# Performance work log

Measured on AMD Instinct MI355X. Metric: run time of the kernel, lower is better.

The kernel has to match this reference:

```python
import jax, jax.numpy as jnp
import numpy as np

B, C = 512, 65536
EPS_COS = 1e-8   # torch cosine_similarity eps
EPS_BCE = 1e-10  # SupGraphLoss denominator eps


def setup_inputs() -> dict:
    key = jax.random.key(0)
    k1, k2, k3 = jax.random.split(key, 3)
    prediction = jax.random.normal(k1, (B, C), dtype=jnp.float32)          # raw logits from the model
    # sparse multi-hot ground-truth labels (yolo_target)
    target = (jax.random.uniform(k2, (B, C)) < 0.02).astype(jnp.float32)
    has_count = jax.random.bernoulli(k3, 0.7, (C,))
    cos_weights = jnp.where(has_count, 0.5, 1.0).astype(jnp.float32)       # CosineOntLoss weights
    bce_weights = has_count.astype(jnp.float32)                            # SupGraphLoss weights
    return {"prediction": prediction, "target": target,
            "cos_weights": cos_weights, "bce_weights": bce_weights}


def _cos_cel_loss(prediction, target, cos_weights, cos_norm_w):
    # CosineOntLoss(result=target, target=prediction):
    # both scaled by weights, cosine similarity along class dim, negative mean.
    a = target * cos_weights       # "target" arg inside CosineOntLoss
    b = prediction * cos_weights   # "result" arg inside CosineOntLoss
    num = jnp.sum(a * b, axis=1)
    na = jnp.sqrt(jnp.sum(a * a, axis=1))
    nb = jnp.sqrt(jnp.sum(b * b, axis=1))
    cos = num / (jnp.maximum(na, EPS_COS) * jnp.maximum(nb, EPS_COS))
    cosine_loss = -jnp.mean(cos)

    # SupGraphLoss(result=target, target=prediction): BCEWithLogits with
    # logits = ground-truth target, soft-target = prediction (faithful to source arg order)
    x = target       # logits
    y = prediction   # bce target
    bce = jnp.maximum(x, 0.0) - x * y + jnp.log1p(jnp.exp(-jnp.abs(x)))  # stable BCEWithLogits
    sub_graph_loss = jnp.sum(bce * cos_norm_w) / (jnp.sum(cos_norm_w) + EPS_BCE)

    return cosine_loss + sub_graph_loss / 10.0


def reference(prediction, target, cos_weights, bce_weights):
    return _cos_cel_loss(prediction, target, cos_weights, bce_weights)
```

## Files before the change

kernel.cpp:

```cpp
#include <hip/hip_runtime.h>

#define B_ROWS   512
#define C_COLS   65536
#define CHUNKS   4
#define T1       256
#define T2       512

__device__ __forceinline__ void wave_reduce4(float& a, float& b, float& c, float& d) {
    #pragma unroll
    for (int off = 32; off >= 1; off >>= 1) {
        a += __shfl_down(a, off);
        b += __shfl_down(b, off);
        c += __shfl_down(c, off);
        d += __shfl_down(d, off);
    }
}

__global__ __launch_bounds__(T1) void coscel_partial(
    const float* __restrict__ pred,
    const float* __restrict__ tgt,
    const float* __restrict__ cw,
    const float* __restrict__ bw,
    float4* __restrict__ ws)
{
    const int blk   = blockIdx.x;
    const int row   = blk >> 2;
    const int chunk = blk & (CHUNKS - 1);
    const int tid   = threadIdx.x;

    const size_t base   = (size_t)row * C_COLS + (size_t)chunk * (C_COLS / CHUNKS);
    const size_t wbase  = (size_t)chunk * (C_COLS / CHUNKS);

    const float4* __restrict__ p4 = (const float4*)(pred + base);
    const float4* __restrict__ t4 = (const float4*)(tgt  + base);
    const float4* __restrict__ w4 = (const float4*)(cw   + wbase);
    const float4* __restrict__ g4 = (const float4*)(bw   + wbase);

    float num = 0.f, a2 = 0.f, b2 = 0.f, bce = 0.f;

    #pragma unroll 4
    for (int i = 0; i < 16; ++i) {
        const int idx = i * T1 + tid;
        const float4 p = p4[idx];
        const float4 t = t4[idx];
        const float4 w = w4[idx];
        const float4 g = g4[idx];

        #define DO_COMP(comp)                                              \
        {                                                                  \
            const float a = t.comp * w.comp;                               \
            const float b = p.comp * w.comp;                               \
            num += a * b;                                                  \
            a2  += a * a;                                                  \
            b2  += b * b;                                                  \
            const float x = t.comp, y = p.comp;                            \
            const float e = __expf(-fabsf(x));                             \
            const float l = __logf(1.0f + e);                              \
            bce += g.comp * (fmaxf(x, 0.0f) - x * y + l);                  \
        }
        DO_COMP(x) DO_COMP(y) DO_COMP(z) DO_COMP(w)
        #undef DO_COMP
    }

    wave_reduce4(num, a2, b2, bce);

    __shared__ float4 sred[T1 / 64];
    const int lane = tid & 63, wid = tid >> 6;
    if (lane == 0) sred[wid] = make_float4(num, a2, b2, bce);
    __syncthreads();
    if (tid == 0) {
        float4 r = sred[0];
        #pragma unroll
        for (int i = 1; i < T1 / 64; ++i) {
            const float4 s = sred[i];
            r.x += s.x; r.y += s.y; r.z += s.z; r.w += s.w;
        }
        ws[blk] = r;
    }
}

__global__ __launch_bounds__(T2) void coscel_final(
    const float4* __restrict__ ws,
    const float* __restrict__ bw,
    float* __restrict__ out)
{
    const int tid = threadIdx.x;

    float num = 0.f, a2 = 0.f, b2 = 0.f, bce = 0.f;
    #pragma unroll
    for (int c = 0; c < CHUNKS; ++c) {
        const float4 v = ws[(size_t)tid * CHUNKS + c];
        num += v.x; a2 += v.y; b2 += v.z; bce += v.w;
    }
    const float na = fmaxf(sqrtf(a2), 1e-8f);
    const float nb = fmaxf(sqrtf(b2), 1e-8f);
    float cosv = num / (na * nb);

    float wsum = 0.f;
    const float4* g4 = (const float4*)bw;
    for (int i = tid; i < C_COLS / 4; i += T2) {
        const float4 g = g4[i];
        wsum += g.x + g.y + g.z + g.w;
    }

    #pragma unroll
    for (int off = 32; off >= 1; off >>= 1) {
        cosv += __shfl_down(cosv, off);
        bce  += __shfl_down(bce,  off);
        wsum += __shfl_down(wsum, off);
    }
    __shared__ float s0[T2 / 64], s1[T2 / 64], s2[T2 / 64];
    const int lane = tid & 63, wid = tid >> 6;
    if (lane == 0) { s0[wid] = cosv; s1[wid] = bce; s2[wid] = wsum; }
    __syncthreads();
    if (tid == 0) {
        float cs = 0.f, bs = 0.f, wss = 0.f;
        #pragma unroll
        for (int i = 0; i < T2 / 64; ++i) { cs += s0[i]; bs += s1[i]; wss += s2[i]; }
        const float cosine_loss   = -(cs / (float)B_ROWS);
        const float sub_graph     = bs / (wss + 1e-10f);
        out[0] = cosine_loss + sub_graph / 10.0f;
    }
}

extern "C" void kernel_launch(void* const* d_in, const int* in_sizes, int n_in,
                              void* d_out, int out_size, void* d_ws, size_t ws_size,
                              hipStream_t stream) {
    const float* pred = (const float*)d_in[0];
    const float* tgt  = (const float*)d_in[1];
    const float* cw   = (const float*)d_in[2];
    const float* bw   = (const float*)d_in[3];
    float* out = (float*)d_out;
    float4* ws = (float4*)d_ws;

    coscel_partial<<<B_ROWS * CHUNKS, T1, 0, stream>>>(pred, tgt, cw, bw, ws);
    coscel_final<<<1, T2, 0, stream>>>(ws, bw, out);
}
```

Baseline: 56.28 us.

## Process four rows per block to reuse weight loads, fold weight sum into partial kernel

Each block now handles a 4-row group over a 4096-column chunk, so the class weight vectors are loaded once and reused across four rows instead of once per row. The bce weight sum is computed by row-group 0 blocks in the partial kernel and written to workspace, removing the serial 64K-element scan from the single-block final kernel. The cost is more registers per thread for four sets of accumulators, and a final kernel that reads 16 partials per row instead of 4.

```diff
diff --git a/kernel.cpp b/kernel.cpp
--- a/kernel.cpp
+++ b/kernel.cpp
@@ -2,9 +2,15 @@
 
 #define B_ROWS   512
 #define C_COLS   65536
-#define CHUNKS   4
+#define BR       4
+#define CCH      4096
+#define NCH      (C_COLS / CCH)
+#define RG       (B_ROWS / BR)
 #define T1       256
+#define ITERS    (CCH / 4 / T1)
 #define T2       512
+
+#define WS_F4_COUNT (B_ROWS * NCH)
 
 __device__ __forceinline__ void wave_reduce4(float& a, float& b, float& c, float& d) {
     #pragma unroll
@@ -23,85 +29,109 @@
     const float* __restrict__ bw,
     float4* __restrict__ ws)
 {
-    const int blk   = blockIdx.x;
-    const int row   = blk >> 2;
-    const int chunk = blk & (CHUNKS - 1);
-    const int tid   = threadIdx.x;
+    const int blk  = blockIdx.x;
+    const int rowg = blk / NCH;
+    const int ch   = blk % NCH;
+    const int tid  = threadIdx.x;
 
-    const size_t base   = (size_t)row * C_COLS + (size_t)chunk * (C_COLS / CHUNKS);
-    const size_t wbase  = (size_t)chunk * (C_COLS / CHUNKS);
+    const int row0 = rowg * BR;
+    const size_t cbase = (size_t)ch * CCH;
 
-    const float4* __restrict__ p4 = (const float4*)(pred + base);
-    const float4* __restrict__ t4 = (const float4*)(tgt  + base);
-    const float4* __restrict__ w4 = (const float4*)(cw   + wbase);
-    const float4* __restrict__ g4 = (const float4*)(bw   + wbase);
+    const float4* __restrict__ w4 = (const float4*)(cw + cbase);
+    const float4* __restrict__ g4 = (const float4*)(bw + cbase);
+    const float4* p4[BR];
+    const float4* t4[BR];
+    #pragma unroll
+    for (int r = 0; r < BR; ++r) {
+        p4[r] = (const float4*)(pred + (size_t)(row0 + r) * C_COLS + cbase);
+        t4[r] = (const float4*)(tgt  + (size_t)(row0 + r) * C_COLS + cbase);
+    }
 
-    float num = 0.f, a2 = 0.f, b2 = 0.f, bce = 0.f;
+    float num[BR], a2[BR], b2[BR], bce[BR];
+    #pragma unroll
+    for (int r = 0; r < BR; ++r) { num[r] = a2[r] = b2[r] = bce[r] = 0.f; }
+    float gsum = 0.f;
 
-    #pragma unroll 4
-    for (int i = 0; i < 16; ++i) {
+    #pragma unroll 2
+    for (int i = 0; i < ITERS; ++i) {
         const int idx = i * T1 + tid;
-        const float4 p = p4[idx];
-        const float4 t = t4[idx];
         const float4 w = w4[idx];
         const float4 g = g4[idx];
+        gsum += g.x + g.y + g.z + g.w;
 
-        #define DO_COMP(comp)                                              \
-        {                                                                  \
-            const float a = t.comp * w.comp;                               \
-            const float b = p.comp * w.comp;                               \
-            num += a * b;                                                  \
-            a2  += a * a;                                                  \
-            b2  += b * b;                                                  \
-            const float x = t.comp, y = p.comp;                            \
-            const float e = __expf(-fabsf(x));                             \
-            const float l = __logf(1.0f + e);                              \
-            bce += g.comp * (fmaxf(x, 0.0f) - x * y + l);                  \
+        float4 pv[BR], tv[BR];
+        #pragma unroll
+        for (int r = 0; r < BR; ++r) { pv[r] = p4[r][idx]; tv[r] = t4[r][idx]; }
+
+        #pragma unroll
+        for (int r = 0; r < BR; ++r) {
+            #define DO_COMP(comp)                                            \
+            {                                                                \
+                const float x = tv[r].comp, y = pv[r].comp;                  \
+                const float a = x * w.comp;                                  \
+                const float b = y * w.comp;                                  \
+                num[r] += a * b;                                             \
+                a2[r]  += a * a;                                             \
+                b2[r]  += b * b;                                             \
+                const float e = __expf(-fabsf(x));                           \
+                const float l = __logf(1.0f + e);                            \
+                bce[r] += g.comp * (fmaxf(x, 0.0f) - x * y + l);             \
+            }
+            DO_COMP(x) DO_COMP(y) DO_COMP(z) DO_COMP(w)
+            #undef DO_COMP
         }
-        DO_COMP(x) DO_COMP(y) DO_COMP(z) DO_COMP(w)
-        #undef DO_COMP
     }
 
-    wave_reduce4(num, a2, b2, bce);
+    #pragma unroll
+    for (int r = 0; r < BR; ++r) wave_reduce4(num[r], a2[r], b2[r], bce[r]);
+    #pragma unroll
+    for (int off = 32; off >= 1; off >>= 1) gsum += __shfl_down(gsum, off);
 
-    __shared__ float4 sred[T1 / 64];
+    __shared__ float4 sred[T1 / 64][BR];
+    __shared__ float  sg[T1 / 64];
     const int lane = tid & 63, wid = tid >> 6;
-    if (lane == 0) sred[wid] = make_float4(num, a2, b2, bce);
+    if (lane == 0) {
+        #pragma unroll
+        for (int r = 0; r < BR; ++r) sred[wid][r] = make_float4(num[r], a2[r], b2[r], bce[r]);
+        sg[wid] = gsum;
+    }
     __syncthreads();
     if (tid == 0) {
-        float4 r = sred[0];
         #pragma unroll
-        for (int i = 1; i < T1 / 64; ++i) {
-            const float4 s = sred[i];
-            r.x += s.x; r.y += s.y; r.z += s.z; r.w += s.w;
+        for (int r = 0; r < BR; ++r) {
+            float4 acc = sred[0][r];
+            #pragma unroll
+            for (int w_ = 1; w_ < T1 / 64; ++w_) {
+                const float4 s = sred[w_][r];
+                acc.x += s.x; acc.y += s.y; acc.z += s.z; acc.w += s.w;
+            }
+            ws[(size_t)(row0 + r) * NCH + ch] = acc;
         }
-        ws[blk] = r;
+        if (rowg == 0) {
+            float gs = sg[0] + sg[1] + sg[2] + sg[3];
+            ((float*)(ws + WS_F4_COUNT))[ch] = gs;
+        }
     }
 }
 
 __global__ __launch_bounds__(T2) void coscel_final(
     const float4* __restrict__ ws,
-    const float* __restrict__ bw,
     float* __restrict__ out)
 {
     const int tid = threadIdx.x;
 
     float num = 0.f, a2 = 0.f, b2 = 0.f, bce = 0.f;
     #pragma unroll
-    for (int c = 0; c < CHUNKS; ++c) {
-        const float4 v = ws[(size_t)tid * CHUNKS + c];
+    for (int c = 0; c < NCH; ++c) {
+        const float4 v = ws[(size_t)tid * NCH + c];
         num += v.x; a2 += v.y; b2 += v.z; bce += v.w;
     }
     const float na = fmaxf(sqrtf(a2), 1e-8f);
     const float nb = fmaxf(sqrtf(b2), 1e-8f);
     float cosv = num / (na * nb);
 
-    float wsum = 0.f;
-    const float4* g4 = (const float4*)bw;
-    for (int i = tid; i < C_COLS / 4; i += T2) {
-        const float4 g = g4[i];
-        wsum += g.x + g.y + g.z + g.w;
-    }
+    const float* wpart = (const float*)(ws + WS_F4_COUNT);
+    float wsum = (tid < NCH) ? wpart[tid] : 0.f;
 
     #pragma unroll
     for (int off = 32; off >= 1; off >>= 1) {
@@ -117,8 +147,8 @@
         float cs = 0.f, bs = 0.f, wss = 0.f;
         #pragma unroll
         for (int i = 0; i < T2 / 64; ++i) { cs += s0[i]; bs += s1[i]; wss += s2[i]; }
-        const float cosine_loss   = -(cs / (float)B_ROWS);
-        const float sub_graph     = bs / (wss + 1e-10f);
+        const float cosine_loss = -(cs / (float)B_ROWS);
+        const float sub_graph   = bs / (wss + 1e-10f);
         out[0] = cosine_loss + sub_graph / 10.0f;
     }
 }
@@ -133,6 +163,6 @@
     float* out = (float*)d_out;
     float4* ws = (float4*)d_ws;
 
-    coscel_partial<<<B_ROWS * CHUNKS, T1, 0, stream>>>(pred, tgt, cw, bw, ws);
-    coscel_final<<<1, T2, 0, stream>>>(ws, bw, out);
+    coscel_partial<<<RG * NCH, T1, 0, stream>>>(pred, tgt, cw, bw, ws);
+    coscel_final<<<1, T2, 0, stream>>>(ws, out);
 }
```

New measurement: 51.13 us. 9.2% less time.
